# Kernel tuning notes

Hardware: AMD Instinct MI355X
Metric: run time of the kernel (lower is better)

## Reference

```python
import jax, jax.numpy as jnp
import numpy as np

RMS_EPS = 1e-5
L2_EPS = 1e-8


def _rms_norm(x, eps=RMS_EPS):
    return x * jax.lax.rsqrt(jnp.mean(x * x, axis=-1, keepdims=True) + eps)


def _l2_norm(x, eps=L2_EPS):
    return jnp.linalg.norm(x, ord=2, axis=-1, keepdims=True) + eps


def setup_inputs() -> dict:
    key = jax.random.key(0)
    kq, kk, kv = jax.random.split(key, 3)
    B, H, S, D = 4, 16, 4096, 64
    Q = jax.random.normal(kq, (B, H, S, D), dtype=jnp.float32)
    K = jax.random.normal(kk, (B, H, S, D), dtype=jnp.float32)
    V = jax.random.normal(kv, (B, H, S, D), dtype=jnp.float32)
    return {"Q": Q, "K": K, "V": V}


def reference(Q, K, V):
    # v_swiglu = SiLU(V) * V
    v_swiglu = jax.nn.silu(V) * V
    # causal cumulative sum over sequence dim
    c = jnp.cumsum(v_swiglu, axis=-2)
    c_n = _rms_norm(c)
    # gating scalar per (b,h,s): ||Q|| + ||K|| + 1
    r = _l2_norm(Q) + _l2_norm(K) + 1.0
    mstate = c_n / r
    # SwiGLU combine: V + SiLU(mstate) * V, then final RMSNorm
    out0 = V + jax.nn.silu(mstate) * V
    return _rms_norm(out0)
```

## Files before the change

kernel.cpp:

```cpp
#include <hip/hip_runtime.h>
#include <math.h>

#define BH 64
#define SEQ 4096
#define DIM 64
#define CHUNK 64
#define NCHUNK (SEQ / CHUNK)

__device__ __forceinline__ float fast_rcp(float x)  { return __builtin_amdgcn_rcpf(x); }
__device__ __forceinline__ float fast_rsqrt(float x){ return __builtin_amdgcn_rsqf(x); }

__device__ __forceinline__ float fast_sigmoid(float x) {
    return fast_rcp(1.0f + __expf(-x));
}

__global__ __launch_bounds__(64) void k_chunksum(const float* __restrict__ V,
                                                 float* __restrict__ P) {
    const int blk  = blockIdx.x;
    const int lane = threadIdx.x;
    const float* vp = V + (size_t)blk * (CHUNK * DIM) + lane;
    float acc = 0.0f;
#pragma unroll 8
    for (int j = 0; j < CHUNK; ++j) {
        float v = vp[j * DIM];
        acc += v * v * fast_sigmoid(v);
    }
    P[(size_t)blk * DIM + lane] = acc;
}

__global__ __launch_bounds__(64) void k_prefix(float* __restrict__ P) {
    const int bh   = blockIdx.x;
    const int lane = threadIdx.x;
    float* p = P + (size_t)bh * (NCHUNK * DIM) + lane;
    float run = 0.0f;
#pragma unroll 4
    for (int ck = 0; ck < NCHUNK; ++ck) {
        float t = p[ck * DIM];
        p[ck * DIM] = run;
        run += t;
    }
}

__global__ __launch_bounds__(64) void k_scan(const float* __restrict__ Q,
                                             const float* __restrict__ K,
                                             const float* __restrict__ V,
                                             const float* __restrict__ P,
                                             float* __restrict__ O) {
    const int blk  = blockIdx.x;
    const int lane = threadIdx.x;
    const size_t base = (size_t)blk * (CHUNK * DIM) + lane;
    const float* qp = Q + base;
    const float* kp = K + base;
    const float* vp = V + base;
    float*       op = O + base;

    float c = P[(size_t)blk * DIM + lane];

    float v = vp[0];
    float q = qp[0];
    float k = kp[0];

    for (int j = 0; j < CHUNK; ++j) {
        const int jn = (j + 1 < CHUNK) ? (j + 1) : (CHUNK - 1);
        float vn = vp[jn * DIM];
        float qn = qp[jn * DIM];
        float kn = kp[jn * DIM];

        float sw = v * v * fast_sigmoid(v);
        c += sw;

        float c2 = c * c;
        float q2 = q * q;
        float k2 = k * k;
#pragma unroll
        for (int m = 1; m < 64; m <<= 1) {
            c2 += __shfl_xor(c2, m);
            q2 += __shfl_xor(q2, m);
            k2 += __shfl_xor(k2, m);
        }

        float rms_c = fast_rsqrt(c2 * (1.0f / 64.0f) + 1e-5f);
        float r     = sqrtf(q2) + sqrtf(k2) + 1.0f;
        float scale = rms_c * fast_rcp(r);

        float m_  = c * scale;
        float sil = m_ * fast_sigmoid(m_);
        float o   = v * (1.0f + sil);

        float o2 = o * o;
#pragma unroll
        for (int m = 1; m < 64; m <<= 1) {
            o2 += __shfl_xor(o2, m);
        }
        float outv = o * fast_rsqrt(o2 * (1.0f / 64.0f) + 1e-5f);
        op[j * DIM] = outv;

        v = vn; q = qn; k = kn;
    }
}

extern "C" void kernel_launch(void* const* d_in, const int* in_sizes, int n_in,
                              void* d_out, int out_size, void* d_ws, size_t ws_size,
                              hipStream_t stream) {
    const float* Q = (const float*)d_in[0];
    const float* K = (const float*)d_in[1];
    const float* V = (const float*)d_in[2];
    float* O = (float*)d_out;
    float* P = (float*)d_ws;

    k_chunksum<<<BH * NCHUNK, 64, 0, stream>>>(V, P);
    k_prefix<<<BH, 64, 0, stream>>>(P);
    k_scan<<<BH * NCHUNK, 64, 0, stream>>>(Q, K, V, P, O);
}
```

Before: 278.0 us.

## Move Q/K norm computation into partials kernel and pack four waves per block

```diff
diff --git a/kernel.cpp b/kernel.cpp
--- a/kernel.cpp
+++ b/kernel.cpp
@@ -4,8 +4,9 @@
 #define BH 64
 #define SEQ 4096
 #define DIM 64
-#define CHUNK 64
+#define CHUNK 32
 #define NCHUNK (SEQ / CHUNK)
+#define WPB 4
 
 __device__ __forceinline__ float fast_rcp(float x)  { return __builtin_amdgcn_rcpf(x); }
 __device__ __forceinline__ float fast_rsqrt(float x){ return __builtin_amdgcn_rsqf(x); }
@@ -14,18 +15,40 @@
     return fast_rcp(1.0f + __expf(-x));
 }
 
-__global__ __launch_bounds__(64) void k_chunksum(const float* __restrict__ V,
-                                                 float* __restrict__ P) {
-    const int blk  = blockIdx.x;
-    const int lane = threadIdx.x;
-    const float* vp = V + (size_t)blk * (CHUNK * DIM) + lane;
-    float acc = 0.0f;
+__global__ __launch_bounds__(256) void k_partials(const float* __restrict__ Q,
+                                                  const float* __restrict__ K,
+                                                  const float* __restrict__ V,
+                                                  float* __restrict__ P,
+                                                  float* __restrict__ R) {
+    const int wave  = threadIdx.x >> 6;
+    const int lane  = threadIdx.x & 63;
+    const int chunk = blockIdx.x * WPB + wave;
+    const size_t base = (size_t)chunk * (CHUNK * DIM) + lane;
+    const float* qp = Q + base;
+    const float* kp = K + base;
+    const float* vp = V + base;
+
+    float acc  = 0.0f;
+    float my_r = 0.0f;
 #pragma unroll 8
     for (int j = 0; j < CHUNK; ++j) {
+        float q = qp[j * DIM];
+        float k = kp[j * DIM];
         float v = vp[j * DIM];
         acc += v * v * fast_sigmoid(v);
+
+        float q2 = q * q;
+        float k2 = k * k;
+#pragma unroll
+        for (int m = 1; m < 64; m <<= 1) {
+            q2 += __shfl_xor(q2, m);
+            k2 += __shfl_xor(k2, m);
+        }
+        float r = sqrtf(q2) + sqrtf(k2) + 1.0f;
+        if (lane == j) my_r = r;
     }
-    P[(size_t)blk * DIM + lane] = acc;
+    P[(size_t)chunk * DIM + lane] = acc;
+    if (lane < CHUNK) R[(size_t)chunk * CHUNK + lane] = my_r;
 }
 
 __global__ __launch_bounds__(64) void k_prefix(float* __restrict__ P) {
@@ -33,7 +56,7 @@
     const int lane = threadIdx.x;
     float* p = P + (size_t)bh * (NCHUNK * DIM) + lane;
     float run = 0.0f;
-#pragma unroll 4
+#pragma unroll 8
     for (int ck = 0; ck < NCHUNK; ++ck) {
         float t = p[ck * DIM];
         p[ck * DIM] = run;
@@ -41,61 +64,41 @@
     }
 }
 
-__global__ __launch_bounds__(64) void k_scan(const float* __restrict__ Q,
-                                             const float* __restrict__ K,
-                                             const float* __restrict__ V,
-                                             const float* __restrict__ P,
-                                             float* __restrict__ O) {
-    const int blk  = blockIdx.x;
-    const int lane = threadIdx.x;
-    const size_t base = (size_t)blk * (CHUNK * DIM) + lane;
-    const float* qp = Q + base;
-    const float* kp = K + base;
+__global__ __launch_bounds__(256) void k_scan(const float* __restrict__ V,
+                                              const float* __restrict__ P,
+                                              const float* __restrict__ R,
+                                              float* __restrict__ O) {
+    const int wave  = threadIdx.x >> 6;
+    const int lane  = threadIdx.x & 63;
+    const int chunk = blockIdx.x * WPB + wave;
+    const size_t base = (size_t)chunk * (CHUNK * DIM) + lane;
     const float* vp = V + base;
     float*       op = O + base;
+    const float* rp = R + (size_t)chunk * CHUNK;
 
-    float c = P[(size_t)blk * DIM + lane];
+    float c = P[(size_t)chunk * DIM + lane];
 
-    float v = vp[0];
-    float q = qp[0];
-    float k = kp[0];
-
+#pragma unroll 8
     for (int j = 0; j < CHUNK; ++j) {
-        const int jn = (j + 1 < CHUNK) ? (j + 1) : (CHUNK - 1);
-        float vn = vp[jn * DIM];
-        float qn = qp[jn * DIM];
-        float kn = kp[jn * DIM];
+        float v = vp[j * DIM];
+        float r = rp[j];
 
         float sw = v * v * fast_sigmoid(v);
         c += sw;
 
         float c2 = c * c;
-        float q2 = q * q;
-        float k2 = k * k;
 #pragma unroll
-        for (int m = 1; m < 64; m <<= 1) {
-            c2 += __shfl_xor(c2, m);
-            q2 += __shfl_xor(q2, m);
-            k2 += __shfl_xor(k2, m);
-        }
+        for (int m = 1; m < 64; m <<= 1) c2 += __shfl_xor(c2, m);
 
         float rms_c = fast_rsqrt(c2 * (1.0f / 64.0f) + 1e-5f);
-        float r     = sqrtf(q2) + sqrtf(k2) + 1.0f;
-        float scale = rms_c * fast_rcp(r);
-
-        float m_  = c * scale;
-        float sil = m_ * fast_sigmoid(m_);
-        float o   = v * (1.0f + sil);
+        float m_    = c * rms_c * fast_rcp(r);
+        float o     = v * (1.0f + m_ * fast_sigmoid(m_));
 
         float o2 = o * o;
 #pragma unroll
-        for (int m = 1; m < 64; m <<= 1) {
-            o2 += __shfl_xor(o2, m);
-        }
-        float outv = o * fast_rsqrt(o2 * (1.0f / 64.0f) + 1e-5f);
-        op[j * DIM] = outv;
+        for (int m = 1; m < 64; m <<= 1) o2 += __shfl_xor(o2, m);
 
-        v = vn; q = qn; k = kn;
+        op[j * DIM] = o * fast_rsqrt(o2 * (1.0f / 64.0f) + 1e-5f);
     }
 }
 
@@ -107,8 +110,10 @@
     const float* V = (const float*)d_in[2];
     float* O = (float*)d_out;
     float* P = (float*)d_ws;
+    float* R = (float*)d_ws + (size_t)BH * NCHUNK * DIM;
 
-    k_chunksum<<<BH * NCHUNK, 64, 0, stream>>>(V, P);
+    const int nchunks = BH * NCHUNK;
+    k_partials<<<nchunks / WPB, 256, 0, stream>>>(Q, K, V, P, R);
     k_prefix<<<BH, 64, 0, stream>>>(P);
-    k_scan<<<BH * NCHUNK, 64, 0, stream>>>(Q, K, V, P, O);
+    k_scan<<<nchunks / WPB, 256, 0, stream>>>(V, P, R, O);
 }
```

New measurement: 253.3 us. 1.1x faster.
